# Kernel optimization log

Hardware: AMD Instinct MI355X
Metric: run time of the kernel (lower is better)

The kernel has to match this reference:

```python
import jax, jax.numpy as jnp
import numpy as np

DIM = 768
N_HEADS = 12
HEAD_DIM = DIM // N_HEADS  # 64
SEQ = 4096
ROPE_THETA = 10000.0  # local layer (layer_id=1)
WINDOW = 128          # local_attention; mask is distance <= WINDOW // 2


def setup_inputs() -> dict:
    key = jax.random.key(0)
    k1, k2, k3 = jax.random.split(key, 3)
    x = jax.random.normal(k1, (1, SEQ, DIM), dtype=jnp.float32)
    position_ids = jnp.arange(SEQ, dtype=jnp.int64 if jax.config.jax_enable_x64 else jnp.int32).reshape(1, SEQ)
    wqkv = jax.random.normal(k2, (3 * DIM, DIM), dtype=jnp.float32) * 0.02
    wo = jax.random.normal(k3, (DIM, DIM), dtype=jnp.float32) * 0.02
    return {"x": x, "position_ids": position_ids, "wqkv": wqkv, "wo": wo}


def _rope_cos_sin(position_ids):
    # inv_freq over even dims, freqs duplicated to full head_dim
    inv_freq = 1.0 / (ROPE_THETA ** (jnp.arange(0, HEAD_DIM, 2, dtype=jnp.float32) / HEAD_DIM))
    pos = position_ids.reshape(-1).astype(jnp.float32)           # [S]
    freqs = pos[:, None] * inv_freq[None, :]                      # [S, hd/2]
    freqs = jnp.concatenate([freqs, freqs], axis=-1)              # [S, hd]
    return jnp.cos(freqs)[None, None], jnp.sin(freqs)[None, None]  # [1,1,S,hd]


def _rotate_half(t):
    h = t.shape[-1] // 2
    return jnp.concatenate([-t[..., h:], t[..., :h]], axis=-1)


def reference(x, position_ids, wqkv, wo):
    bsz, seq_len, _ = x.shape
    qkv = jnp.einsum("bsd,ed->bse", x, wqkv)                      # [B,S,3*dim]
    qkv = qkv.reshape(bsz, seq_len, 3, N_HEADS, HEAD_DIM)
    qkv = jnp.transpose(qkv, (0, 3, 2, 1, 4))                      # [B,H,3,S,hd]
    q, k, v = qkv[:, :, 0], qkv[:, :, 1], qkv[:, :, 2]             # [B,H,S,hd]

    cos, sin = _rope_cos_sin(position_ids)
    q = q * cos + _rotate_half(q) * sin
    k = k * cos + _rotate_half(k) * sin

    scale = HEAD_DIM ** -0.5
    scores = jnp.einsum("bhqd,bhkd->bhqk", q, k) * scale           # [B,H,S,S]

    # sliding-window mask: |i - j| <= WINDOW // 2
    idx = jnp.arange(seq_len)
    dist = jnp.abs(idx[None, :] - idx[:, None])                    # [S,S]
    window_mask = dist <= (WINDOW // 2)
    scores = jnp.where(window_mask[None, None], scores, -jnp.inf)

    attn = jax.nn.softmax(scores, axis=-1)
    out = jnp.einsum("bhqk,bhkd->bhqd", attn, v)                   # [B,H,S,hd]
    out = jnp.transpose(out, (0, 2, 1, 3)).reshape(bsz, seq_len, DIM)
    out = jnp.einsum("bsd,ed->bse", out, wo)
    return out
```

## Files before the change

kernel.cpp:

```cpp
#include <hip/hip_runtime.h>
#include <math.h>

#define SEQ 4096
#define DIM 768
#define NH 12
#define HD 64
#define QKV_N 2304
#define HALF_WIN 64

typedef __attribute__((ext_vector_type(8))) short bf16x8;
typedef __attribute__((ext_vector_type(4))) float floatx4;

__device__ __forceinline__ unsigned short f2bf(float f) {
    unsigned u = __float_as_uint(f);
    unsigned r = (u + 0x7fffu + ((u >> 16) & 1u)) >> 16;
    return (unsigned short)r;
}

__device__ __forceinline__ void gld16(const void* g, void* l) {
    __builtin_amdgcn_global_load_lds(
        (const __attribute__((address_space(1))) unsigned*)g,
        (__attribute__((address_space(3))) unsigned*)l, 16, 0, 0);
}

__device__ __forceinline__ void fast_sc(float x, float* s, float* c) {
    float r = x * 0.15915494309189535f;
    r = r - floorf(r);
    *s = __builtin_amdgcn_sinf(r);
    *c = __builtin_amdgcn_cosf(r);
}

__global__ __launch_bounds__(256) void cast3_bf16(const float* __restrict__ x,
                                                  const float* __restrict__ wqkv,
                                                  const float* __restrict__ wo,
                                                  unsigned short* __restrict__ dst,
                                                  int nx4, int nw4, int ntot4) {
    int i = blockIdx.x * 256 + threadIdx.x;
    if (i >= ntot4) return;
    const float4* src;
    int off;
    if (i < nx4)            { src = (const float4*)x;    off = i; }
    else if (i < nx4 + nw4) { src = (const float4*)wqkv; off = i - nx4; }
    else                    { src = (const float4*)wo;   off = i - nx4 - nw4; }
    float4 v = src[off];
    ushort4 r;
    r.x = f2bf(v.x); r.y = f2bf(v.y); r.z = f2bf(v.z); r.w = f2bf(v.w);
    *(ushort4*)(dst + (size_t)i * 4) = r;
}

__global__ __launch_bounds__(512, 4) void gemm_qkv_rope(const unsigned short* __restrict__ A,
                                                        const unsigned short* __restrict__ B,
                                                        unsigned short* __restrict__ qr,
                                                        unsigned short* __restrict__ kr,
                                                        unsigned short* __restrict__ vt) {
    __shared__ __align__(16) short smem[32768];
    const int t  = threadIdx.x;
    const int wv = t >> 6, ln = t & 63;
    const int wm = wv >> 2;
    const int wn = wv & 3;
    const int bm0 = blockIdx.y * 128;
    const int bn0 = blockIdx.x * 128;
    const int lrow = ln >> 3;
    const int lu   = ln & 7;
    const int frow = ln & 15;
    const int q    = ln >> 4;
    const int K = DIM;
    const int nbase = (wn >> 1) * 64 + (wn & 1) * 16;

    const unsigned short* gptr[4];
    int loff[4];
#pragma unroll
    for (int i = 0; i < 4; i++) {
        int idx = wv * 4 + i;
        int c   = (idx < 16) ? idx : idx - 16;
        int row = c * 8 + lrow;
        int g   = (lu ^ (row & 7)) << 3;
        if (idx < 16) {
            gptr[i] = A + (size_t)(bm0 + row) * K + g;
            loff[i] = c * 512;
        } else {
            gptr[i] = B + (size_t)(bn0 + row) * K + g;
            loff[i] = 8192 + c * 512;
        }
    }

    floatx4 acc[4][2];
#pragma unroll
    for (int i = 0; i < 4; i++)
#pragma unroll
        for (int j = 0; j < 2; j++) acc[i][j] = (floatx4){0.f, 0.f, 0.f, 0.f};

#pragma unroll
    for (int i = 0; i < 4; i++) gld16(gptr[i], (void*)(smem + loff[i]));
    __syncthreads();

    int cur = 0;
    for (int it = 0; it < 12; it++) {
        if (it + 1 < 12) {
            int nb = cur ^ 1;
            int k0n = (it + 1) * 64;
#pragma unroll
            for (int i = 0; i < 4; i++)
                gld16(gptr[i] + k0n, (void*)(smem + nb * 16384 + loff[i]));
        }
        short* As = smem + cur * 16384;
        short* Bs = As + 8192;
#pragma unroll
        for (int ks = 0; ks < 2; ks++) {
            bf16x8 af[4], bfr[2];
#pragma unroll
            for (int mt = 0; mt < 4; mt++) {
                int ra = wm * 64 + mt * 16 + frow;
                af[mt] = *(const bf16x8*)&As[ra * 64 + (((ks * 4 + q) ^ (ra & 7)) << 3)];
            }
#pragma unroll
            for (int nt = 0; nt < 2; nt++) {
                int rb = nbase + nt * 32 + frow;
                bfr[nt] = *(const bf16x8*)&Bs[rb * 64 + (((ks * 4 + q) ^ (rb & 7)) << 3)];
            }
#pragma unroll
            for (int mt = 0; mt < 4; mt++)
#pragma unroll
                for (int nt = 0; nt < 2; nt++)
                    acc[mt][nt] = __builtin_amdgcn_mfma_f32_16x16x32_bf16(
                        af[mt], bfr[nt], acc[mt][nt], 0, 0, 0);
        }
        __syncthreads();
        cur ^= 1;
    }

    const int cn = frow;
    const int part = (bn0 >= 1536) ? 2 : (bn0 >= 768 ? 1 : 0);

    if (part < 2) {
        const int di = (wn & 1) * 16 + cn;
        const int h  = (bn0 - part * 768 + (wn >> 1) * 64) >> 6;
        unsigned short* dst = (part == 0 ? qr : kr) + (size_t)h * SEQ * HD;
        const float invf = exp2f(-(float)di * 0.4152410118609203f);
#pragma unroll
        for (int mt = 0; mt < 4; mt++) {
            const int sbase = bm0 + wm * 64 + mt * 16 + q * 4;
#pragma unroll
            for (int r = 0; r < 4; r++) {
                float ss = (float)(sbase + r);
                float sn, cs;
                fast_sc(ss * invf, &sn, &cs);
                float lo = acc[mt][0][r] * cs - acc[mt][1][r] * sn;
                float hi = acc[mt][1][r] * cs + acc[mt][0][r] * sn;
                unsigned short* p = dst + (size_t)(sbase + r) * HD + di;
                p[0]  = f2bf(lo);
                p[32] = f2bf(hi);
            }
        }
    } else {
        short* vstage = smem;
#pragma unroll
        for (int nt = 0; nt < 2; nt++) {
#pragma unroll
            for (int mt = 0; mt < 4; mt++) {
                int d    = nbase + nt * 32 + cn;
                int sloc = wm * 64 + mt * 16 + q * 4;
                ushort4 pk;
                pk.x = f2bf(acc[mt][nt][0]);
                pk.y = f2bf(acc[mt][nt][1]);
                pk.z = f2bf(acc[mt][nt][2]);
                pk.w = f2bf(acc[mt][nt][3]);
                *(ushort4*)&vstage[d * 136 + sloc] = pk;
            }
        }
        __syncthreads();
        const int dr = t >> 2, su = (t & 3) * 32;
        uint4 v0 = *(const uint4*)&vstage[dr * 136 + su];
        uint4 v1 = *(const uint4*)&vstage[dr * 136 + su + 8];
        uint4 v2 = *(const uint4*)&vstage[dr * 136 + su + 16];
        uint4 v3 = *(const uint4*)&vstage[dr * 136 + su + 24];
        unsigned short* vp = vt + (size_t)(bn0 - 1536 + dr) * SEQ + bm0 + su;
        *(uint4*)(vp)      = v0;
        *(uint4*)(vp + 8)  = v1;
        *(uint4*)(vp + 16) = v2;
        *(uint4*)(vp + 24) = v3;
    }
}

__global__ __launch_bounds__(256) void gemm_out(const unsigned short* __restrict__ A,
                                                const unsigned short* __restrict__ B,
                                                float* __restrict__ C,
                                                int M, int N, int K) {
    __shared__ __align__(16) short smem[16384];
    const int t  = threadIdx.x;
    const int wv = t >> 6, ln = t & 63;
    const int wm = wv >> 1, wn = wv & 1;
    const int bm0 = blockIdx.y * 64;
    const int bn0 = blockIdx.x * 64;
    const int lrow = ln >> 3;
    const int lu   = ln & 7;
    const int frow = ln & 15;
    const int q    = ln >> 4;

    const unsigned short* gptr[4];
    int loff[4];
#pragma unroll
    for (int i = 0; i < 4; i++) {
        int idx = wv * 4 + i;
        int c   = (idx < 8) ? idx : idx - 8;
        int row = c * 8 + lrow;
        int g   = (lu ^ (row & 7)) << 3;
        if (idx < 8) {
            gptr[i] = A + (size_t)(bm0 + row) * K + g;
            loff[i] = c * 512;
        } else {
            gptr[i] = B + (size_t)(bn0 + row) * K + g;
            loff[i] = 4096 + c * 512;
        }
    }

    floatx4 acc[2][2];
#pragma unroll
    for (int i = 0; i < 2; i++)
#pragma unroll
        for (int j = 0; j < 2; j++) acc[i][j] = (floatx4){0.f, 0.f, 0.f, 0.f};

#pragma unroll
    for (int i = 0; i < 4; i++) gld16(gptr[i], (void*)(smem + loff[i]));
    __syncthreads();

    int cur = 0;
    const int NIT = K / 64;
    for (int it = 0; it < NIT; it++) {
        if (it + 1 < NIT) {
            int nb = cur ^ 1;
            int k0n = (it + 1) * 64;
#pragma unroll
            for (int i = 0; i < 4; i++)
                gld16(gptr[i] + k0n, (void*)(smem + nb * 8192 + loff[i]));
        }
        short* As = smem + cur * 8192;
        short* Bs = As + 4096;
#pragma unroll
        for (int ks = 0; ks < 2; ks++) {
            bf16x8 af[2], bfr[2];
#pragma unroll
            for (int mt = 0; mt < 2; mt++) {
                int ra = wm * 32 + mt * 16 + frow;
                af[mt] = *(const bf16x8*)&As[ra * 64 + (((ks * 4 + q) ^ (ra & 7)) << 3)];
            }
#pragma unroll
            for (int nt = 0; nt < 2; nt++) {
                int rb = wn * 32 + nt * 16 + frow;
                bfr[nt] = *(const bf16x8*)&Bs[rb * 64 + (((ks * 4 + q) ^ (rb & 7)) << 3)];
            }
#pragma unroll
            for (int mt = 0; mt < 2; mt++)
#pragma unroll
                for (int nt = 0; nt < 2; nt++)
                    acc[mt][nt] = __builtin_amdgcn_mfma_f32_16x16x32_bf16(
                        af[mt], bfr[nt], acc[mt][nt], 0, 0, 0);
        }
        __syncthreads();
        cur ^= 1;
    }

    const int cn = ln & 15;
    const int rb4 = (ln >> 4) * 4;
#pragma unroll
    for (int mt = 0; mt < 2; mt++) {
#pragma unroll
        for (int nt = 0; nt < 2; nt++) {
            floatx4 v = acc[mt][nt];
            float* cp = C + (size_t)(bm0 + wm * 32 + mt * 16 + rb4) * N +
                        bn0 + wn * 32 + nt * 16 + cn;
#pragma unroll
            for (int r = 0; r < 4; r++) cp[(size_t)r * N] = v[r];
        }
    }
}

__global__ __launch_bounds__(512) void attn_mfma(const unsigned short* __restrict__ Q,
                                                 const unsigned short* __restrict__ K,
                                                 const unsigned short* __restrict__ Vt,
                                                 unsigned short* __restrict__ Out) {
    __shared__ __align__(16) short lds[24576];
    short* Pb = lds + 16384;
    const int t  = threadIdx.x;
    const int wv = t >> 6, ln = t & 63;
    const int h  = blockIdx.x, qs = blockIdx.y * 128;
    const int frow = ln & 15, qd = ln >> 4;
    const int rl = ln >> 3, uu = ln & 7;
    const unsigned short* Qh = Q + (size_t)h * SEQ * HD;
    const unsigned short* Kh = K + (size_t)h * SEQ * HD;
    const unsigned short* Vh = Vt + (size_t)h * HD * SEQ;

    const unsigned short* qp = Qh + (size_t)(qs + wv * 16 + frow) * HD;
    bf16x8 af0 = *(const bf16x8*)(qp + qd * 8);
    bf16x8 af1 = *(const bf16x8*)(qp + (qd + 4) * 8);

    floatx4 accO[4];
#pragma unroll
    for (int i = 0; i < 4; i++) accO[i] = (floatx4){0.f, 0.f, 0.f, 0.f};
    float m_r[4] = {-1e30f, -1e30f, -1e30f, -1e30f};
    float l_r[4] = {0.f, 0.f, 0.f, 0.f};

    const int qlo = wv * 16;
    const int srow = wv * 8 + rl;
    const int sg   = uu ^ ((srow + (srow >> 3)) & 7);

    {
        const int kb0 = qs - 64;
        const int kbc = kb0 < 0 ? 0 : (kb0 > SEQ - 64 ? SEQ - 64 : kb0);
        gld16(Kh + (size_t)(kbc + srow) * HD + sg * 8, (void*)(lds + wv * 512));
        gld16(Vh + (size_t)srow * SEQ + kbc + sg * 8, (void*)(lds + 4096 + wv * 512));
    }
    __syncthreads();

    int cur = 0;
    for (int c = 0; c < 4; c++) {
        if (c + 1 < 4) {
            const int kb1 = qs - 64 + (c + 1) * 64;
            const int kbc1 = kb1 < 0 ? 0 : (kb1 > SEQ - 64 ? SEQ - 64 : kb1);
            short* nb = lds + (cur ^ 1) * 8192;
            gld16(Kh + (size_t)(kbc1 + srow) * HD + sg * 8, (void*)(nb + wv * 512));
            gld16(Vh + (size_t)srow * SEQ + kbc1 + sg * 8, (void*)(nb + 4096 + wv * 512));
        }
        short* Ks  = lds + cur * 8192;
        short* Vts = Ks + 4096;
        const int kb = qs - 64 + c * 64;

        const int klo0 = c * 64 - 64;
        bool live_kt[4];
        bool any_live = false;
#pragma unroll
        for (int kt = 0; kt < 4; kt++) {
            int d0 = qlo - (klo0 + kt * 16);
            live_kt[kt] = (d0 <= 64) && (d0 >= -64);
            any_live = any_live || live_kt[kt];
        }

        if (any_live) {
            float sv[4][4];
            float cm[4] = {-1e30f, -1e30f, -1e30f, -1e30f};
#pragma unroll
            for (int kt = 0; kt < 4; kt++) {
                if (live_kt[kt]) {
                    int brow = kt * 16 + frow;
                    int bz = (brow + (brow >> 3)) & 7;
                    bf16x8 b0 = *(const bf16x8*)&Ks[brow * 64 + ((qd ^ bz) << 3)];
                    bf16x8 b1 = *(const bf16x8*)&Ks[brow * 64 + (((qd + 4) ^ bz) << 3)];
                    floatx4 z = (floatx4){0.f, 0.f, 0.f, 0.f};
                    z = __builtin_amdgcn_mfma_f32_16x16x32_bf16(af0, b0, z, 0, 0, 0);
                    z = __builtin_amdgcn_mfma_f32_16x16x32_bf16(af1, b1, z, 0, 0, 0);
                    int gk = kb + kt * 16 + frow;
#pragma unroll
                    for (int r = 0; r < 4; r++) {
                        int gq = qs + wv * 16 + qd * 4 + r;
                        int dd = gq - gk;
                        bool valid = (gk >= 0) && (gk < SEQ) &&
                                     (dd <= HALF_WIN) && (dd >= -HALF_WIN);
                        float x = valid ? z[r] * 0.125f : -1e30f;
                        sv[kt][r] = x;
                        cm[r] = fmaxf(cm[r], x);
                    }
                } else {
#pragma unroll
                    for (int r = 0; r < 4; r++) sv[kt][r] = -1e30f;
                }
            }
#pragma unroll
            for (int off = 1; off < 16; off <<= 1)
#pragma unroll
                for (int r = 0; r < 4; r++)
                    cm[r] = fmaxf(cm[r], __shfl_xor(cm[r], off, 64));
            float al[4], ls[4];
#pragma unroll
            for (int r = 0; r < 4; r++) {
                float mn = fmaxf(m_r[r], cm[r]);
                al[r] = __expf(m_r[r] - mn);
                m_r[r] = mn;
                ls[r] = 0.f;
            }
            const int qrb = wv * 16 + qd * 4;
#pragma unroll
            for (int kt = 0; kt < 4; kt++) {
                int klocal = kt * 16 + frow;
                int ku = klocal >> 3;
                if (live_kt[kt]) {
#pragma unroll
                    for (int r = 0; r < 4; r++) {
                        float p = (sv[kt][r] > -1e29f) ? __expf(sv[kt][r] - m_r[r]) : 0.f;
                        ls[r] += p;
                        int qrow = qrb + r;
                        int pz = (qrow + (qrow >> 3)) & 7;
                        Pb[qrow * 64 + ((ku ^ pz) << 3) + (klocal & 7)] = (short)f2bf(p);
                    }
                } else {
#pragma unroll
                    for (int r = 0; r < 4; r++) {
                        int qrow = qrb + r;
                        int pz = (qrow + (qrow >> 3)) & 7;
                        Pb[qrow * 64 + ((ku ^ pz) << 3) + (klocal & 7)] = 0;
                    }
                }
            }
#pragma unroll
            for (int off = 1; off < 16; off <<= 1)
#pragma unroll
                for (int r = 0; r < 4; r++) ls[r] += __shfl_xor(ls[r], off, 64);
#pragma unroll
            for (int r = 0; r < 4; r++) l_r[r] = l_r[r] * al[r] + ls[r];
#pragma unroll
            for (int dt = 0; dt < 4; dt++)
#pragma unroll
                for (int r = 0; r < 4; r++) accO[dt][r] *= al[r];

            const int prow = wv * 16 + frow;
            const int pz2 = (prow + (prow >> 3)) & 7;
            bf16x8 pa0 = *(const bf16x8*)&Pb[prow * 64 + ((qd ^ pz2) << 3)];
            bf16x8 pa1 = *(const bf16x8*)&Pb[prow * 64 + (((qd + 4) ^ pz2) << 3)];
#pragma unroll
            for (int dt = 0; dt < 4; dt++) {
                int vrow = dt * 16 + frow;
                int vz = (vrow + (vrow >> 3)) & 7;
                bf16x8 v0 = *(const bf16x8*)&Vts[vrow * 64 + ((qd ^ vz) << 3)];
                bf16x8 v1 = *(const bf16x8*)&Vts[vrow * 64 + (((qd + 4) ^ vz) << 3)];
                accO[dt] = __builtin_amdgcn_mfma_f32_16x16x32_bf16(pa0, v0, accO[dt], 0, 0, 0);
                accO[dt] = __builtin_amdgcn_mfma_f32_16x16x32_bf16(pa1, v1, accO[dt], 0, 0, 0);
            }
        }
        __syncthreads();
        cur ^= 1;
    }

    short* Ob = lds;
    float linv[4];
#pragma unroll
    for (int r = 0; r < 4; r++) linv[r] = 1.0f / l_r[r];
#pragma unroll
    for (int dt = 0; dt < 4; dt++)
#pragma unroll
        for (int r = 0; r < 4; r++) {
            int qrow = wv * 16 + qd * 4 + r;
            int dcol = dt * 16 + frow;
            Ob[qrow * 72 + dcol] = (short)f2bf(accO[dt][r] * linv[r]);
        }
    __syncthreads();
    const int orow = t >> 2, og = (t & 3) * 16;
    uint4 a = *(const uint4*)&Ob[orow * 72 + og];
    uint4 b = *(const uint4*)&Ob[orow * 72 + og + 8];
    unsigned short* op = Out + (size_t)(qs + orow) * DIM + h * HD + og;
    *(uint4*)(op)     = a;
    *(uint4*)(op + 8) = b;
}

extern "C" void kernel_launch(void* const* d_in, const int* in_sizes, int n_in,
                              void* d_out, int out_size, void* d_ws, size_t ws_size,
                              hipStream_t stream) {
    const float* x    = (const float*)d_in[0];
    const float* wqkv = (const float*)d_in[2];
    const float* wo   = (const float*)d_in[3];
    float* out = (float*)d_out;

    unsigned short* q_r  = (unsigned short*)d_ws;
    unsigned short* k_r  = q_r + (size_t)NH * SEQ * HD;
    unsigned short* v_t  = k_r + (size_t)NH * SEQ * HD;
    unsigned short* x_bf = v_t + (size_t)NH * SEQ * HD;
    unsigned short* wqkv_bf = x_bf + (size_t)SEQ * DIM;
    unsigned short* wo_bf   = wqkv_bf + (size_t)QKV_N * DIM;
    unsigned short* attn_bf = wo_bf + (size_t)DIM * DIM;

    const int nx4 = SEQ * DIM / 4;
    const int nw4 = QKV_N * DIM / 4;
    const int no4 = DIM * DIM / 4;
    const int ntot4 = nx4 + nw4 + no4;

    cast3_bf16<<<dim3((ntot4 + 255) / 256), 256, 0, stream>>>(
        x, wqkv, wo, x_bf, nx4, nw4, ntot4);
    gemm_qkv_rope<<<dim3(QKV_N / 128, SEQ / 128), 512, 0, stream>>>(
        x_bf, wqkv_bf, q_r, k_r, v_t);
    attn_mfma<<<dim3(NH, SEQ / 128), 512, 0, stream>>>(
        q_r, k_r, v_t, attn_bf);
    gemm_out<<<dim3(DIM / 64, SEQ / 64), 256, 0, stream>>>(
        attn_bf, wo_bf, out, SEQ, DIM, DIM);
}
```

Before: 128.8 us.

## Halve M-tile of QKV GEMM and attention, add XCD-aware block remapping

The QKV GEMM goes from 128x128 tiles with 8 waves to 64x128 tiles with 4 waves, and attention goes from 128-query to 64-query blocks with 4 waves and 3 key chunks, doubling the grid sizes. All three GEMM and attention kernels remap block IDs so consecutive blocks on the same XCD share rows, which should improve L2 reuse. This is meant to raise occupancy and balance across CUs and cut wasted key chunks. In exchange, each block reuses less data and does more redundant K/V loading per query.

Result: faster. 119.6 us, median of 2 (-7.1%).

```diff
diff --git a/kernel.cpp b/kernel.cpp
--- a/kernel.cpp
+++ b/kernel.cpp
@@ -7,6 +7,7 @@
 #define HD 64
 #define QKV_N 2304
 #define HALF_WIN 64
+#define QBLK 64
 
 typedef __attribute__((ext_vector_type(8))) short bf16x8;
 typedef __attribute__((ext_vector_type(4))) float floatx4;
@@ -48,39 +49,41 @@
     *(ushort4*)(dst + (size_t)i * 4) = r;
 }
 
-__global__ __launch_bounds__(512, 4) void gemm_qkv_rope(const unsigned short* __restrict__ A,
+__global__ __launch_bounds__(256, 3) void gemm_qkv_rope(const unsigned short* __restrict__ A,
                                                         const unsigned short* __restrict__ B,
                                                         unsigned short* __restrict__ qr,
                                                         unsigned short* __restrict__ kr,
                                                         unsigned short* __restrict__ vt) {
-    __shared__ __align__(16) short smem[32768];
+    __shared__ __align__(16) short smem[24576];
     const int t  = threadIdx.x;
     const int wv = t >> 6, ln = t & 63;
-    const int wm = wv >> 2;
-    const int wn = wv & 3;
-    const int bm0 = blockIdx.y * 128;
-    const int bn0 = blockIdx.x * 128;
+    const int o    = blockIdx.y * 18 + blockIdx.x;
+    const int xcd  = o & 7;
+    const int j    = o >> 3;
+    const int bm0  = (xcd * 8 + (j & 7)) * 64;
+    const int bn0  = (j >> 3) * 128;
     const int lrow = ln >> 3;
     const int lu   = ln & 7;
     const int frow = ln & 15;
     const int q    = ln >> 4;
     const int K = DIM;
+    const int wn = wv;
     const int nbase = (wn >> 1) * 64 + (wn & 1) * 16;
 
-    const unsigned short* gptr[4];
-    int loff[4];
-#pragma unroll
-    for (int i = 0; i < 4; i++) {
-        int idx = wv * 4 + i;
-        int c   = (idx < 16) ? idx : idx - 16;
+    const unsigned short* gptr[6];
+    int loff[6];
+#pragma unroll
+    for (int i = 0; i < 6; i++) {
+        int idx = wv * 6 + i;
+        int c   = (idx < 8) ? idx : idx - 8;
         int row = c * 8 + lrow;
         int g   = (lu ^ (row & 7)) << 3;
-        if (idx < 16) {
+        if (idx < 8) {
             gptr[i] = A + (size_t)(bm0 + row) * K + g;
             loff[i] = c * 512;
         } else {
             gptr[i] = B + (size_t)(bn0 + row) * K + g;
-            loff[i] = 8192 + c * 512;
+            loff[i] = 4096 + c * 512;
         }
     }
 
@@ -88,10 +91,10 @@
 #pragma unroll
     for (int i = 0; i < 4; i++)
 #pragma unroll
-        for (int j = 0; j < 2; j++) acc[i][j] = (floatx4){0.f, 0.f, 0.f, 0.f};
-
-#pragma unroll
-    for (int i = 0; i < 4; i++) gld16(gptr[i], (void*)(smem + loff[i]));
+        for (int j2 = 0; j2 < 2; j2++) acc[i][j2] = (floatx4){0.f, 0.f, 0.f, 0.f};
+
+#pragma unroll
+    for (int i = 0; i < 6; i++) gld16(gptr[i], (void*)(smem + loff[i]));
     __syncthreads();
 
     int cur = 0;
@@ -100,17 +103,17 @@
             int nb = cur ^ 1;
             int k0n = (it + 1) * 64;
 #pragma unroll
-            for (int i = 0; i < 4; i++)
-                gld16(gptr[i] + k0n, (void*)(smem + nb * 16384 + loff[i]));
-        }
-        short* As = smem + cur * 16384;
-        short* Bs = As + 8192;
+            for (int i = 0; i < 6; i++)
+                gld16(gptr[i] + k0n, (void*)(smem + nb * 12288 + loff[i]));
+        }
+        short* As = smem + cur * 12288;
+        short* Bs = As + 4096;
 #pragma unroll
         for (int ks = 0; ks < 2; ks++) {
             bf16x8 af[4], bfr[2];
 #pragma unroll
             for (int mt = 0; mt < 4; mt++) {
-                int ra = wm * 64 + mt * 16 + frow;
+                int ra = mt * 16 + frow;
                 af[mt] = *(const bf16x8*)&As[ra * 64 + (((ks * 4 + q) ^ (ra & 7)) << 3)];
             }
 #pragma unroll
@@ -139,7 +142,7 @@
         const float invf = exp2f(-(float)di * 0.4152410118609203f);
 #pragma unroll
         for (int mt = 0; mt < 4; mt++) {
-            const int sbase = bm0 + wm * 64 + mt * 16 + q * 4;
+            const int sbase = bm0 + mt * 16 + q * 4;
 #pragma unroll
             for (int r = 0; r < 4; r++) {
                 float ss = (float)(sbase + r);
@@ -159,21 +162,21 @@
 #pragma unroll
             for (int mt = 0; mt < 4; mt++) {
                 int d    = nbase + nt * 32 + cn;
-                int sloc = wm * 64 + mt * 16 + q * 4;
+                int sloc = mt * 16 + q * 4;
                 ushort4 pk;
                 pk.x = f2bf(acc[mt][nt][0]);
                 pk.y = f2bf(acc[mt][nt][1]);
                 pk.z = f2bf(acc[mt][nt][2]);
                 pk.w = f2bf(acc[mt][nt][3]);
-                *(ushort4*)&vstage[d * 136 + sloc] = pk;
+                *(ushort4*)&vstage[d * 72 + sloc] = pk;
             }
         }
         __syncthreads();
-        const int dr = t >> 2, su = (t & 3) * 32;
-        uint4 v0 = *(const uint4*)&vstage[dr * 136 + su];
-        uint4 v1 = *(const uint4*)&vstage[dr * 136 + su + 8];
-        uint4 v2 = *(const uint4*)&vstage[dr * 136 + su + 16];
-        uint4 v3 = *(const uint4*)&vstage[dr * 136 + su + 24];
+        const int dr = t >> 1, su = (t & 1) * 32;
+        uint4 v0 = *(const uint4*)&vstage[dr * 72 + su];
+        uint4 v1 = *(const uint4*)&vstage[dr * 72 + su + 8];
+        uint4 v2 = *(const uint4*)&vstage[dr * 72 + su + 16];
+        uint4 v3 = *(const uint4*)&vstage[dr * 72 + su + 24];
         unsigned short* vp = vt + (size_t)(bn0 - 1536 + dr) * SEQ + bm0 + su;
         *(uint4*)(vp)      = v0;
         *(uint4*)(vp + 8)  = v1;
@@ -190,8 +193,11 @@
     const int t  = threadIdx.x;
     const int wv = t >> 6, ln = t & 63;
     const int wm = wv >> 1, wn = wv & 1;
-    const int bm0 = blockIdx.y * 64;
-    const int bn0 = blockIdx.x * 64;
+    const int o   = blockIdx.y * 12 + blockIdx.x;
+    const int xcd = o & 7;
+    const int j   = o >> 3;
+    const int bm0 = (xcd * 8 + (j & 7)) * 64;
+    const int bn0 = (j >> 3) * 64;
     const int lrow = ln >> 3;
     const int lu   = ln & 7;
     const int frow = ln & 15;
@@ -218,7 +224,7 @@
 #pragma unroll
     for (int i = 0; i < 2; i++)
 #pragma unroll
-        for (int j = 0; j < 2; j++) acc[i][j] = (floatx4){0.f, 0.f, 0.f, 0.f};
+        for (int j2 = 0; j2 < 2; j2++) acc[i][j2] = (floatx4){0.f, 0.f, 0.f, 0.f};
 
 #pragma unroll
     for (int i = 0; i < 4; i++) gld16(gptr[i], (void*)(smem + loff[i]));
@@ -275,15 +281,18 @@
     }
 }
 
-__global__ __launch_bounds__(512) void attn_mfma(const unsigned short* __restrict__ Q,
+__global__ __launch_bounds__(256) void attn_mfma(const unsigned short* __restrict__ Q,
                                                  const unsigned short* __restrict__ K,
                                                  const unsigned short* __restrict__ Vt,
                                                  unsigned short* __restrict__ Out) {
-    __shared__ __align__(16) short lds[24576];
+    __shared__ __align__(16) short lds[20480];
     short* Pb = lds + 16384;
     const int t  = threadIdx.x;
     const int wv = t >> 6, ln = t & 63;
-    const int h  = blockIdx.x, qs = blockIdx.y * 128;
+    const int o = blockIdx.y * 12 + blockIdx.x;
+    const int L = (o & 7) * 96 + (o >> 3);
+    const int h  = L % 12;
+    const int qs = (L / 12) * QBLK;
     const int frow = ln & 15, qd = ln >> 4;
     const int rl = ln >> 3, uu = ln & 7;
     const unsigned short* Qh = Q + (size_t)h * SEQ * HD;
@@ -301,25 +310,31 @@
     float l_r[4] = {0.f, 0.f, 0.f, 0.f};
 
     const int qlo = wv * 16;
-    const int srow = wv * 8 + rl;
-    const int sg   = uu ^ ((srow + (srow >> 3)) & 7);
+    const int srow0 = wv * 16 + rl;
+    const int srow1 = srow0 + 8;
+    const int sg0 = uu ^ ((srow0 + (srow0 >> 3)) & 7);
+    const int sg1 = uu ^ ((srow1 + (srow1 >> 3)) & 7);
 
     {
         const int kb0 = qs - 64;
         const int kbc = kb0 < 0 ? 0 : (kb0 > SEQ - 64 ? SEQ - 64 : kb0);
-        gld16(Kh + (size_t)(kbc + srow) * HD + sg * 8, (void*)(lds + wv * 512));
-        gld16(Vh + (size_t)srow * SEQ + kbc + sg * 8, (void*)(lds + 4096 + wv * 512));
+        gld16(Kh + (size_t)(kbc + srow0) * HD + sg0 * 8, (void*)(lds + (wv * 16) * 64));
+        gld16(Kh + (size_t)(kbc + srow1) * HD + sg1 * 8, (void*)(lds + (wv * 16 + 8) * 64));
+        gld16(Vh + (size_t)srow0 * SEQ + kbc + sg0 * 8, (void*)(lds + 4096 + (wv * 16) * 64));
+        gld16(Vh + (size_t)srow1 * SEQ + kbc + sg1 * 8, (void*)(lds + 4096 + (wv * 16 + 8) * 64));
     }
     __syncthreads();
 
     int cur = 0;
-    for (int c = 0; c < 4; c++) {
-        if (c + 1 < 4) {
+    for (int c = 0; c < 3; c++) {
+        if (c + 1 < 3) {
             const int kb1 = qs - 64 + (c + 1) * 64;
             const int kbc1 = kb1 < 0 ? 0 : (kb1 > SEQ - 64 ? SEQ - 64 : kb1);
             short* nb = lds + (cur ^ 1) * 8192;
-            gld16(Kh + (size_t)(kbc1 + srow) * HD + sg * 8, (void*)(nb + wv * 512));
-            gld16(Vh + (size_t)srow * SEQ + kbc1 + sg * 8, (void*)(nb + 4096 + wv * 512));
+            gld16(Kh + (size_t)(kbc1 + srow0) * HD + sg0 * 8, (void*)(nb + (wv * 16) * 64));
+            gld16(Kh + (size_t)(kbc1 + srow1) * HD + sg1 * 8, (void*)(nb + (wv * 16 + 8) * 64));
+            gld16(Vh + (size_t)srow0 * SEQ + kbc1 + sg0 * 8, (void*)(nb + 4096 + (wv * 16) * 64));
+            gld16(Vh + (size_t)srow1 * SEQ + kbc1 + sg1 * 8, (void*)(nb + 4096 + (wv * 16 + 8) * 64));
         }
         short* Ks  = lds + cur * 8192;
         short* Vts = Ks + 4096;
@@ -473,9 +488,9 @@
 
     cast3_bf16<<<dim3((ntot4 + 255) / 256), 256, 0, stream>>>(
         x, wqkv, wo, x_bf, nx4, nw4, ntot4);
-    gemm_qkv_rope<<<dim3(QKV_N / 128, SEQ / 128), 512, 0, stream>>>(
+    gemm_qkv_rope<<<dim3(QKV_N / 128, SEQ / 64), 256, 0, stream>>>(
         x_bf, wqkv_bf, q_r, k_r, v_t);
-    attn_mfma<<<dim3(NH, SEQ / 128), 512, 0, stream>>>(
+    attn_mfma<<<dim3(NH, SEQ / QBLK), 256, 0, stream>>>(
         q_r, k_r, v_t, attn_bf);
     gemm_out<<<dim3(DIM / 64, SEQ / 64), 256, 0, stream>>>(
         attn_bf, wo_bf, out, SEQ, DIM, DIM);
```
